# Optimization experiments

Hardware: AMD Instinct MI355X
Metric: run time of the kernel (lower is better)

## Reference

```python
import jax, jax.numpy as jnp
import numpy as np
from jax import lax

SIGMA = 3.0
AP_CUT = 15


def _gauss_kernel(sigma, truncate=4.0):
    r = int(truncate * sigma + 0.5)
    x = np.arange(-r, r + 1, dtype=np.float32)
    k = np.exp(-0.5 * (x / sigma) ** 2)
    return jnp.asarray(k / k.sum()), r

KERN, RAD = _gauss_kernel(SIGMA)


def _smooth(f):
    """Separable Gaussian smoothing; circular on y (DV), replicate on x (AP).
    f: [..., Y, X] -> same shape."""
    lead = f.shape[:-2]
    Y, X = f.shape[-2:]
    g = f.reshape((-1, 1, Y, X))
    g = jnp.pad(g, ((0, 0), (0, 0), (RAD, RAD), (0, 0)), mode='wrap')
    g = jnp.pad(g, ((0, 0), (0, 0), (0, 0), (RAD, RAD)), mode='edge')
    ky = KERN.reshape(1, 1, -1, 1)
    kx = KERN.reshape(1, 1, 1, -1)
    g = lax.conv_general_dilated(g, ky, (1, 1), 'VALID')
    g = lax.conv_general_dilated(g, kx, (1, 1), 'VALID')
    return g.reshape(lead + (Y, X))


def _gradient(f):
    """Covariant gradient: Gaussian smooth then central differences.
    Returns [..., Y, X, 2] with index 0 = d/dy (circular), 1 = d/dx (replicate)."""
    g = _smooth(f)
    dy = 0.5 * (jnp.roll(g, -1, axis=-2) - jnp.roll(g, 1, axis=-2))
    gp = jnp.pad(g, [(0, 0)] * (g.ndim - 1) + [(1, 1)], mode='edge')
    dx = 0.5 * (gp[..., 2:] - gp[..., :-2])
    return jnp.stack([dy, dx], axis=-1)


def _postprocess(f):
    f = f.at[..., :AP_CUT].set(0.0)
    f = f.at[..., -AP_CUT:].set(0.0)
    return _smooth(f)


def setup_inputs() -> dict:
    key = jax.random.key(0)
    k1, k2 = jax.random.split(key)
    Y, X = 1024, 2048
    y = 0.1 * jax.random.normal(k1, (5, Y, X), dtype=jnp.float32)
    v = 0.1 * jax.random.normal(k2, (2, Y, X), dtype=jnp.float32)
    return {"y": y, "v": v}


def reference(y, v):
    Y, X = y.shape[-2:]
    # InputProcessor.transform: split state into 2x2 tensor m and scalar s
    m = y[:4].reshape(2, 2, Y, X)
    s = y[4]

    # get_velocity: left-right symmetrization (flip DV axis, negate y-component)
    v_lr = jnp.flip(v, axis=-2)
    v_lr = v_lr.at[0].multiply(-1.0)
    v = 0.5 * (v + v_lr)

    d1_m = _gradient(m)          # [2,2,Y,X,2]
    d1_s = _gradient(s)          # [Y,X,2]
    d1_v = _gradient(v)          # [2,Y,X,2]

    sdot = -jnp.einsum('iyx,yxi->yx', v, d1_s)

    T = jnp.transpose(d1_v, (0, 3, 1, 2))       # iyxj -> ijyx
    Tt = jnp.transpose(T, (1, 0, 2, 3))
    O = -0.5 * (T - Tt)                         # vorticity
    E = 0.5 * (T + Tt)                          # strain rate

    lhs = jnp.einsum('kyx,ijyxk->ijyx', v, d1_m)
    lhs = lhs + jnp.einsum('ikyx,kjyx->ijyx', O, m)
    lhs = lhs - jnp.einsum('ikyx,kjyx->ijyx', m, O)

    # rhs_eCad reaction terms
    trm = jnp.einsum('kkyx->yx', m)
    trE = jnp.einsum('kkyx->yx', E)
    gamma_dv = jnp.array([[1.0, 0.0], [0.0, 0.0]], dtype=y.dtype)[..., None, None]
    rhs = -(0.11 - 0.099 * s) * m
    rhs = rhs + (0.767 + 0.055 * s) * m * trE
    rhs = rhs + (0.732 - 0.59 * s) * trm * m
    rhs = rhs + (0.069 - 0.048 * s) * trm * gamma_dv

    mdot = _postprocess(-lhs + rhs)
    sdot = _postprocess(sdot)

    # inverse_transform: stack back into 5-channel state derivative
    return jnp.concatenate([mdot.reshape(4, Y, X), sdot[None]], axis=0)
```

## Files before the change

### kernel.cpp

```cpp
#include <hip/hip_runtime.h>
#include <math.h>

#define Y_ 1024
#define X_ 2048
#define YX_ (Y_*X_)
#define RAD_ 12
#define NT_ 25
#define ND_ 27
#define APC_ 15
#define PAD_ 16

struct W25 { float w[NT_]; };
struct D27 { float d[ND_]; };

__global__ __launch_bounds__(256) void ksmooth_y7c(
    const float* __restrict__ yin, const float* __restrict__ vin,
    float* __restrict__ out, W25 W)
{
  const int id = blockIdx.x;
  const int w  = (id & 7) * 112 + (id >> 3);
  const int yg = w % 64, xh = (w / 64) & 1, z = w / 128;
  const int y0 = yg * 16;
  const int xo = xh * 1024 + threadIdx.x * 4;

  float4 acc[16];
#pragma unroll
  for (int j = 0; j < 16; ++j) acc[j] = make_float4(0.f, 0.f, 0.f, 0.f);

  if (z < 5) {
    const float* base = yin + z * YX_;
#pragma unroll
    for (int g = 0; g < 4; ++g) {
      float4 b[10];
#pragma unroll
      for (int i = 0; i < 10; ++i) {
        const int r = (y0 - RAD_ + 10*g + i + Y_) & (Y_ - 1);
        b[i] = *(const float4*)(base + r * X_ + xo);
      }
#pragma unroll
      for (int i = 0; i < 10; ++i) {
        const int t = 10*g + i;
#pragma unroll
        for (int j = 0; j < 16; ++j) {
          const int k = t - j;
          if (k >= 0 && k < NT_) {
            const float wk = W.w[k];
            acc[j].x += wk * b[i].x; acc[j].y += wk * b[i].y;
            acc[j].z += wk * b[i].z; acc[j].w += wk * b[i].w;
          }
        }
      }
    }
  } else {
    const int   c   = z - 5;
    const float sgn = (c == 0) ? -1.f : 1.f;
    const float* base = vin + c * YX_;
#pragma unroll
    for (int g = 0; g < 8; ++g) {
      float4 a5[5], b5[5];
#pragma unroll
      for (int i = 0; i < 5; ++i) {
        const int r = (y0 - RAD_ + 5*g + i + Y_) & (Y_ - 1);
        a5[i] = *(const float4*)(base + r * X_ + xo);
        b5[i] = *(const float4*)(base + (Y_ - 1 - r) * X_ + xo);
      }
#pragma unroll
      for (int i = 0; i < 5; ++i) {
        const int t = 5*g + i;
        float4 val;
        val.x = 0.5f * (a5[i].x + sgn * b5[i].x);
        val.y = 0.5f * (a5[i].y + sgn * b5[i].y);
        val.z = 0.5f * (a5[i].z + sgn * b5[i].z);
        val.w = 0.5f * (a5[i].w + sgn * b5[i].w);
#pragma unroll
        for (int j = 0; j < 16; ++j) {
          const int k = t - j;
          if (k >= 0 && k < NT_) {
            const float wk = W.w[k];
            acc[j].x += wk * val.x; acc[j].y += wk * val.y;
            acc[j].z += wk * val.z; acc[j].w += wk * val.w;
          }
        }
      }
    }
  }
#pragma unroll
  for (int j = 0; j < 16; ++j)
    *(float4*)(out + z * YX_ + (y0 + j) * X_ + xo) = acc[j];
}

__device__ __forceinline__ void stage_row(
    float (&slot)[4][264], const float* __restrict__ src, int tid)
{
  float4 v = *(const float4*)(src + 4 * tid);
  slot[0][tid] = v.x; slot[1][tid] = v.y; slot[2][tid] = v.z; slot[3][tid] = v.w;
  if (tid < 8) {
    float4 v2 = *(const float4*)(src + 1024 + 4 * tid);
    slot[0][256+tid] = v2.x; slot[1][256+tid] = v2.y;
    slot[2][256+tid] = v2.z; slot[3][256+tid] = v2.w;
  }
}

__device__ __forceinline__ void conv_lds(
    const float (&L)[3][4][264], int tid, const W25& W, const D27& D,
    float dX[4], float dY[4])
{
#pragma unroll
  for (int j = 0; j < 4; ++j) { dX[j] = 0.f; dY[j] = 0.f; }
#pragma unroll
  for (int i = 3; i <= 33; ++i) {
    const float v = L[1][i & 3][tid + (i >> 2)];
#pragma unroll
    for (int j = 0; j < 4; ++j) {
      const int k = i - 3 - j;
      if (k >= 0 && k < ND_) dX[j] += D.d[k] * v;
    }
  }
#pragma unroll
  for (int i = 4; i <= 31; ++i) {
    const float u = L[2][i & 3][tid + (i >> 2)];
    const float d = L[0][i & 3][tid + (i >> 2)];
    const float dv = 0.5f * (u - d);
#pragma unroll
    for (int j = 0; j < 4; ++j) {
      const int k = i - 4 - j;
      if (k >= 0 && k < NT_) dY[j] += W.w[k] * dv;
    }
  }
}

__global__ __launch_bounds__(256, 4) void kfused_lds3(
    const float* __restrict__ gY,
    const float* __restrict__ yin,
    const float* __restrict__ vin,
    float* __restrict__ B,
    W25 W, D27 D)
{
  __shared__ float lds[3][4][264];
  const int tid = threadIdx.x;
  const int id  = blockIdx.x;
  const int w   = (id & 7) * 256 + (id >> 3);
  const int yy  = w & (Y_ - 1);
  const int xh  = w >> 10;
  const int xb  = xh * 1024;
  const int x0  = xb + 4 * tid;
  const int yu  = (yy + 1) & (Y_ - 1);
  const int yd  = (yy - 1) & (Y_ - 1);

  float v0[4], v1[4];
  {
    float4 a = *(const float4*)(vin + 0 * YX_ + yy * X_ + x0);
    float4 b = *(const float4*)(vin + 0 * YX_ + (Y_ - 1 - yy) * X_ + x0);
    float4 c = *(const float4*)(vin + 1 * YX_ + yy * X_ + x0);
    float4 d = *(const float4*)(vin + 1 * YX_ + (Y_ - 1 - yy) * X_ + x0);
    v0[0] = 0.5f*(a.x-b.x); v0[1] = 0.5f*(a.y-b.y);
    v0[2] = 0.5f*(a.z-b.z); v0[3] = 0.5f*(a.w-b.w);
    v1[0] = 0.5f*(c.x+d.x); v1[1] = 0.5f*(c.y+d.y);
    v1[2] = 0.5f*(c.z+d.z); v1[3] = 0.5f*(c.w+d.w);
  }

  float dXa[4], dYa[4], w_[4], trE[4];
  float ac0[4], ac1[4], ac2[4], ac3[4], ac4[4];

  {
    const float* b5 = gY + 5 * YX_;
    stage_row(lds[0], b5 + yd * X_ + xb - 16, tid);
    stage_row(lds[1], b5 + yy * X_ + xb - 16, tid);
    stage_row(lds[2], b5 + yu * X_ + xb - 16, tid);
  }
  __syncthreads();

#pragma unroll 1
  for (int ci = 0; ci < 7; ++ci) {
    float dX[4], dY[4];
    conv_lds(lds, tid, W, D, dX, dY);
    switch (ci) {
      case 0:
#pragma unroll
        for (int j = 0; j < 4; ++j) { dXa[j] = dX[j]; dYa[j] = dY[j]; }
        break;
      case 1:
#pragma unroll
        for (int j = 0; j < 4; ++j) {
          w_[j]  = -0.5f * (dXa[j] - dY[j]);
          trE[j] = dYa[j] + dX[j];
        }
        break;
      case 2:
#pragma unroll
        for (int j = 0; j < 4; ++j) ac0[j] = v0[j]*dY[j] + v1[j]*dX[j];
        break;
      case 3:
#pragma unroll
        for (int j = 0; j < 4; ++j) ac1[j] = v0[j]*dY[j] + v1[j]*dX[j];
        break;
      case 4:
#pragma unroll
        for (int j = 0; j < 4; ++j) ac2[j] = v0[j]*dY[j] + v1[j]*dX[j];
        break;
      case 5:
#pragma unroll
        for (int j = 0; j < 4; ++j) ac3[j] = v0[j]*dY[j] + v1[j]*dX[j];
        break;
      default:
#pragma unroll
        for (int j = 0; j < 4; ++j) ac4[j] = v0[j]*dY[j] + v1[j]*dX[j];
        break;
    }
    if (ci < 6) {
      __syncthreads();
      const int nch = (ci == 0) ? 6 : ci - 1;
      const float* bn = gY + nch * YX_;
      stage_row(lds[0], bn + yd * X_ + xb - 16, tid);
      stage_row(lds[1], bn + yy * X_ + xb - 16, tid);
      stage_row(lds[2], bn + yu * X_ + xb - 16, tid);
      __syncthreads();
    }
  }

  float rm[5][4];
#pragma unroll
  for (int zc = 0; zc < 5; ++zc) {
    float4 t = *(const float4*)(yin + zc * YX_ + yy * X_ + x0);
    rm[zc][0] = t.x; rm[zc][1] = t.y; rm[zc][2] = t.z; rm[zc][3] = t.w;
  }

  float o[5][4];
#pragma unroll
  for (int j = 0; j < 4; ++j) {
    const float m00r = rm[0][j], m01r = rm[1][j], m10r = rm[2][j], m11r = rm[3][j];
    const float sr   = rm[4][j];
    const float wj   = w_[j];
    const float trm  = m00r + m11r;

    const float lhs00 = ac0[j] + wj * (m10r + m01r);
    const float lhs01 = ac1[j] + wj * (m11r - m00r);
    const float lhs10 = ac2[j] + wj * (m11r - m00r);
    const float lhs11 = ac3[j] - wj * (m01r + m10r);

    const float f  = -(0.11f - 0.099f * sr)
                   + (0.767f + 0.055f * sr) * trE[j]
                   + (0.732f - 0.59f  * sr) * trm;
    const float cd = (0.069f - 0.048f * sr) * trm;
    const float sd = -ac4[j];

    const int   xg   = x0 + j;
    const float mask = (xg < APC_ || xg >= X_ - APC_) ? 0.f : 1.f;
    o[0][j] = mask * (f * m00r + cd - lhs00);
    o[1][j] = mask * (f * m01r      - lhs01);
    o[2][j] = mask * (f * m10r      - lhs10);
    o[3][j] = mask * (f * m11r      - lhs11);
    o[4][j] = mask * sd;
  }
#pragma unroll
  for (int zc = 0; zc < 5; ++zc)
    *(float4*)(B + zc * YX_ + yy * X_ + x0) =
        make_float4(o[zc][0], o[zc][1], o[zc][2], o[zc][3]);
}

__global__ __launch_bounds__(256) void kxsmooth(
    const float* __restrict__ in, float* __restrict__ out, W25 W)
{
  const int z  = blockIdx.z;
  const int yy = blockIdx.y;
  const int x0 = (blockIdx.x * 256 + threadIdx.x) * 4;
  const float* row = in + z * YX_ + yy * X_;

  float buf[28];
  if (x0 >= RAD_ && x0 + 4 + RAD_ <= X_) {
#pragma unroll
    for (int i = 0; i < 7; ++i) {
      float4 t = *(const float4*)(row + x0 - RAD_ + 4 * i);
      buf[4*i+0] = t.x; buf[4*i+1] = t.y; buf[4*i+2] = t.z; buf[4*i+3] = t.w;
    }
  } else {
#pragma unroll
    for (int i = 0; i < 28; ++i) {
      int xx = x0 - RAD_ + i;
      xx = xx < 0 ? 0 : (xx > X_ - 1 ? X_ - 1 : xx);
      buf[i] = row[xx];
    }
  }
  float a0 = 0.f, a1 = 0.f, a2 = 0.f, a3 = 0.f;
#pragma unroll
  for (int t = 0; t < NT_; ++t) {
    const float wk = W.w[t];
    a0 += wk * buf[t + 0];
    a1 += wk * buf[t + 1];
    a2 += wk * buf[t + 2];
    a3 += wk * buf[t + 3];
  }
  *(float4*)(out + z * YX_ + yy * X_ + x0) = make_float4(a0, a1, a2, a3);
}

__global__ __launch_bounds__(256) void ksmooth_y5c(
    const float* __restrict__ in, float* __restrict__ out, W25 W)
{
  const int id = blockIdx.x;
  const int w  = (id & 7) * 80 + (id >> 3);
  const int yg = w % 64, xh = (w / 64) & 1, z = w / 128;
  const int y0 = yg * 16;
  const int xo = xh * 1024 + threadIdx.x * 4;
  const float* base = in + z * YX_;

  float4 acc[16];
#pragma unroll
  for (int j = 0; j < 16; ++j) acc[j] = make_float4(0.f, 0.f, 0.f, 0.f);

#pragma unroll
  for (int g = 0; g < 4; ++g) {
    float4 b[10];
#pragma unroll
    for (int i = 0; i < 10; ++i) {
      const int r = (y0 - RAD_ + 10*g + i + Y_) & (Y_ - 1);
      b[i] = *(const float4*)(base + r * X_ + xo);
    }
#pragma unroll
    for (int i = 0; i < 10; ++i) {
      const int t = 10*g + i;
#pragma unroll
      for (int j = 0; j < 16; ++j) {
        const int k = t - j;
        if (k >= 0 && k < NT_) {
          const float wk = W.w[k];
          acc[j].x += wk * b[i].x; acc[j].y += wk * b[i].y;
          acc[j].z += wk * b[i].z; acc[j].w += wk * b[i].w;
        }
      }
    }
  }
#pragma unroll
  for (int j = 0; j < 16; ++j)
    *(float4*)(out + z * YX_ + (y0 + j) * X_ + xo) = acc[j];
}

extern "C" void kernel_launch(void* const* d_in, const int* in_sizes, int n_in,
                              void* d_out, int out_size, void* d_ws, size_t ws_size,
                              hipStream_t stream)
{
  const float* yin = (const float*)d_in[0];
  const float* vin = (const float*)d_in[1];
  float* out = (float*)d_out;

  float* gY = (float*)d_ws + PAD_;
  float* B  = gY + 7 * (size_t)YX_;
  float* C  = gY;

  W25 W; D27 D;
  double wd[NT_], s = 0.0;
  for (int i = 0; i < NT_; ++i) {
    const double x = i - RAD_;
    wd[i] = exp(-0.5 * (x / 3.0) * (x / 3.0));
    s += wd[i];
  }
  for (int i = 0; i < NT_; ++i) W.w[i] = (float)(wd[i] / s);
  for (int t = 0; t < ND_; ++t) {
    const double a = (t - 2 >= 0 && t - 2 < NT_) ? wd[t - 2] / s : 0.0;
    const double b = (t < NT_) ? wd[t] / s : 0.0;
    D.d[t] = (float)(0.5 * (a - b));
  }

  ksmooth_y7c<<<896,  256, 0, stream>>>(yin, vin, gY, W);
  kfused_lds3<<<2048, 256, 0, stream>>>(gY, yin, vin, B, W, D);
  kxsmooth   <<<dim3(2, 1024, 5), 256, 0, stream>>>(B, C, W);
  ksmooth_y5c<<<640,  256, 0, stream>>>(C, out, W);
}
```

Measured before the change: 226.3 us.

## Fuse x-direction smoothing into gradient kernel with halo recompute and double-buffered LDS

```diff
diff --git a/kernel.cpp b/kernel.cpp
--- a/kernel.cpp
+++ b/kernel.cpp
@@ -8,7 +8,7 @@
 #define NT_ 25
 #define ND_ 27
 #define APC_ 15
-#define PAD_ 16
+#define PAD_ 32
 
 struct W25 { float w[NT_]; };
 struct D27 { float d[ND_]; };
@@ -89,27 +89,24 @@
     *(float4*)(out + z * YX_ + (y0 + j) * X_ + xo) = acc[j];
 }
 
-__device__ __forceinline__ void stage_row(
-    float (&slot)[4][264], const float* __restrict__ src, int tid)
-{
-  float4 v = *(const float4*)(src + 4 * tid);
-  slot[0][tid] = v.x; slot[1][tid] = v.y; slot[2][tid] = v.z; slot[3][tid] = v.w;
-  if (tid < 8) {
-    float4 v2 = *(const float4*)(src + 1024 + 4 * tid);
-    slot[0][256+tid] = v2.x; slot[1][256+tid] = v2.y;
-    slot[2][256+tid] = v2.z; slot[3][256+tid] = v2.w;
-  }
-}
-
-__device__ __forceinline__ void conv_lds(
-    const float (&L)[3][4][264], int tid, const W25& W, const D27& D,
+__device__ __forceinline__ void stage_row2(
+    float (&slot)[4][272], const float* __restrict__ src, int tid)
+{
+  if (tid < 270) {
+    float4 v = *(const float4*)(src + 4 * tid);
+    slot[0][tid] = v.x; slot[1][tid] = v.y; slot[2][tid] = v.z; slot[3][tid] = v.w;
+  }
+}
+
+__device__ __forceinline__ void conv_lds2(
+    const float (&L)[3][4][272], int g, const W25& W, const D27& D,
     float dX[4], float dY[4])
 {
 #pragma unroll
   for (int j = 0; j < 4; ++j) { dX[j] = 0.f; dY[j] = 0.f; }
 #pragma unroll
   for (int i = 3; i <= 33; ++i) {
-    const float v = L[1][i & 3][tid + (i >> 2)];
+    const float v = L[1][i & 3][g + (i >> 2)];
 #pragma unroll
     for (int j = 0; j < 4; ++j) {
       const int k = i - 3 - j;
@@ -118,8 +115,8 @@
   }
 #pragma unroll
   for (int i = 4; i <= 31; ++i) {
-    const float u = L[2][i & 3][tid + (i >> 2)];
-    const float d = L[0][i & 3][tid + (i >> 2)];
+    const float u = L[2][i & 3][g + (i >> 2)];
+    const float d = L[0][i & 3][g + (i >> 2)];
     const float dv = 0.5f * (u - d);
 #pragma unroll
     for (int j = 0; j < 4; ++j) {
@@ -129,30 +126,33 @@
   }
 }
 
-__global__ __launch_bounds__(256, 4) void kfused_lds3(
+__global__ __launch_bounds__(320, 3) void kfused_x(
     const float* __restrict__ gY,
     const float* __restrict__ yin,
     const float* __restrict__ vin,
-    float* __restrict__ B,
+    float* __restrict__ Bx,
     W25 W, D27 D)
 {
-  __shared__ float lds[3][4][264];
+  __shared__ float lds[2][3][4][272];
+  __shared__ float ox[5][4][264];
   const int tid = threadIdx.x;
   const int id  = blockIdx.x;
   const int w   = (id & 7) * 256 + (id >> 3);
   const int yy  = w & (Y_ - 1);
   const int xh  = w >> 10;
   const int xb  = xh * 1024;
-  const int x0  = xb + 4 * tid;
+  const int x0  = xb - 12 + 4 * tid;
   const int yu  = (yy + 1) & (Y_ - 1);
   const int yd  = (yy - 1) & (Y_ - 1);
+  const bool act = (tid < 262);
+  const int xr  = x0 < 0 ? 0 : (x0 > X_ - 4 ? X_ - 4 : x0);
 
   float v0[4], v1[4];
   {
-    float4 a = *(const float4*)(vin + 0 * YX_ + yy * X_ + x0);
-    float4 b = *(const float4*)(vin + 0 * YX_ + (Y_ - 1 - yy) * X_ + x0);
-    float4 c = *(const float4*)(vin + 1 * YX_ + yy * X_ + x0);
-    float4 d = *(const float4*)(vin + 1 * YX_ + (Y_ - 1 - yy) * X_ + x0);
+    float4 a = *(const float4*)(vin + 0 * YX_ + yy * X_ + xr);
+    float4 b = *(const float4*)(vin + 0 * YX_ + (Y_ - 1 - yy) * X_ + xr);
+    float4 c = *(const float4*)(vin + 1 * YX_ + yy * X_ + xr);
+    float4 d = *(const float4*)(vin + 1 * YX_ + (Y_ - 1 - yy) * X_ + xr);
     v0[0] = 0.5f*(a.x-b.x); v0[1] = 0.5f*(a.y-b.y);
     v0[2] = 0.5f*(a.z-b.z); v0[3] = 0.5f*(a.w-b.w);
     v1[0] = 0.5f*(c.x+d.x); v1[1] = 0.5f*(c.y+d.y);
@@ -164,16 +164,24 @@
 
   {
     const float* b5 = gY + 5 * YX_;
-    stage_row(lds[0], b5 + yd * X_ + xb - 16, tid);
-    stage_row(lds[1], b5 + yy * X_ + xb - 16, tid);
-    stage_row(lds[2], b5 + yu * X_ + xb - 16, tid);
+    stage_row2(lds[0][0], b5 + yd * X_ + xb - 28, tid);
+    stage_row2(lds[0][1], b5 + yy * X_ + xb - 28, tid);
+    stage_row2(lds[0][2], b5 + yu * X_ + xb - 28, tid);
   }
   __syncthreads();
 
 #pragma unroll 1
   for (int ci = 0; ci < 7; ++ci) {
+    if (ci < 6) {
+      const int nch = (ci == 0) ? 6 : ci - 1;
+      const float* bn = gY + nch * YX_;
+      float (&nb)[3][4][272] = lds[(ci + 1) & 1];
+      stage_row2(nb[0], bn + yd * X_ + xb - 28, tid);
+      stage_row2(nb[1], bn + yy * X_ + xb - 28, tid);
+      stage_row2(nb[2], bn + yu * X_ + xb - 28, tid);
+    }
     float dX[4], dY[4];
-    conv_lds(lds, tid, W, D, dX, dY);
+    conv_lds2(lds[ci & 1], act ? tid : 0, W, D, dX, dY);
     switch (ci) {
       case 0:
 #pragma unroll
@@ -207,90 +215,67 @@
         for (int j = 0; j < 4; ++j) ac4[j] = v0[j]*dY[j] + v1[j]*dX[j];
         break;
     }
-    if (ci < 6) {
-      __syncthreads();
-      const int nch = (ci == 0) ? 6 : ci - 1;
-      const float* bn = gY + nch * YX_;
-      stage_row(lds[0], bn + yd * X_ + xb - 16, tid);
-      stage_row(lds[1], bn + yy * X_ + xb - 16, tid);
-      stage_row(lds[2], bn + yu * X_ + xb - 16, tid);
-      __syncthreads();
-    }
-  }
-
-  float rm[5][4];
-#pragma unroll
-  for (int zc = 0; zc < 5; ++zc) {
-    float4 t = *(const float4*)(yin + zc * YX_ + yy * X_ + x0);
-    rm[zc][0] = t.x; rm[zc][1] = t.y; rm[zc][2] = t.z; rm[zc][3] = t.w;
-  }
-
-  float o[5][4];
-#pragma unroll
-  for (int j = 0; j < 4; ++j) {
-    const float m00r = rm[0][j], m01r = rm[1][j], m10r = rm[2][j], m11r = rm[3][j];
-    const float sr   = rm[4][j];
-    const float wj   = w_[j];
-    const float trm  = m00r + m11r;
-
-    const float lhs00 = ac0[j] + wj * (m10r + m01r);
-    const float lhs01 = ac1[j] + wj * (m11r - m00r);
-    const float lhs10 = ac2[j] + wj * (m11r - m00r);
-    const float lhs11 = ac3[j] - wj * (m01r + m10r);
-
-    const float f  = -(0.11f - 0.099f * sr)
-                   + (0.767f + 0.055f * sr) * trE[j]
-                   + (0.732f - 0.59f  * sr) * trm;
-    const float cd = (0.069f - 0.048f * sr) * trm;
-    const float sd = -ac4[j];
-
-    const int   xg   = x0 + j;
-    const float mask = (xg < APC_ || xg >= X_ - APC_) ? 0.f : 1.f;
-    o[0][j] = mask * (f * m00r + cd - lhs00);
-    o[1][j] = mask * (f * m01r      - lhs01);
-    o[2][j] = mask * (f * m10r      - lhs10);
-    o[3][j] = mask * (f * m11r      - lhs11);
-    o[4][j] = mask * sd;
-  }
-#pragma unroll
-  for (int zc = 0; zc < 5; ++zc)
-    *(float4*)(B + zc * YX_ + yy * X_ + x0) =
-        make_float4(o[zc][0], o[zc][1], o[zc][2], o[zc][3]);
-}
-
-__global__ __launch_bounds__(256) void kxsmooth(
-    const float* __restrict__ in, float* __restrict__ out, W25 W)
-{
-  const int z  = blockIdx.z;
-  const int yy = blockIdx.y;
-  const int x0 = (blockIdx.x * 256 + threadIdx.x) * 4;
-  const float* row = in + z * YX_ + yy * X_;
-
-  float buf[28];
-  if (x0 >= RAD_ && x0 + 4 + RAD_ <= X_) {
-#pragma unroll
-    for (int i = 0; i < 7; ++i) {
-      float4 t = *(const float4*)(row + x0 - RAD_ + 4 * i);
-      buf[4*i+0] = t.x; buf[4*i+1] = t.y; buf[4*i+2] = t.z; buf[4*i+3] = t.w;
-    }
-  } else {
-#pragma unroll
-    for (int i = 0; i < 28; ++i) {
-      int xx = x0 - RAD_ + i;
-      xx = xx < 0 ? 0 : (xx > X_ - 1 ? X_ - 1 : xx);
-      buf[i] = row[xx];
-    }
-  }
-  float a0 = 0.f, a1 = 0.f, a2 = 0.f, a3 = 0.f;
-#pragma unroll
-  for (int t = 0; t < NT_; ++t) {
-    const float wk = W.w[t];
-    a0 += wk * buf[t + 0];
-    a1 += wk * buf[t + 1];
-    a2 += wk * buf[t + 2];
-    a3 += wk * buf[t + 3];
-  }
-  *(float4*)(out + z * YX_ + yy * X_ + x0) = make_float4(a0, a1, a2, a3);
+    __syncthreads();
+  }
+
+  if (act) {
+    float rm[5][4];
+#pragma unroll
+    for (int zc = 0; zc < 5; ++zc) {
+      float4 t = *(const float4*)(yin + zc * YX_ + yy * X_ + xr);
+      rm[zc][0] = t.x; rm[zc][1] = t.y; rm[zc][2] = t.z; rm[zc][3] = t.w;
+    }
+#pragma unroll
+    for (int j = 0; j < 4; ++j) {
+      const float m00r = rm[0][j], m01r = rm[1][j], m10r = rm[2][j], m11r = rm[3][j];
+      const float sr   = rm[4][j];
+      const float wj   = w_[j];
+      const float trm  = m00r + m11r;
+
+      const float lhs00 = ac0[j] + wj * (m10r + m01r);
+      const float lhs01 = ac1[j] + wj * (m11r - m00r);
+      const float lhs10 = ac2[j] + wj * (m11r - m00r);
+      const float lhs11 = ac3[j] - wj * (m01r + m10r);
+
+      const float f  = -(0.11f - 0.099f * sr)
+                     + (0.767f + 0.055f * sr) * trE[j]
+                     + (0.732f - 0.59f  * sr) * trm;
+      const float cd = (0.069f - 0.048f * sr) * trm;
+      const float sd = -ac4[j];
+
+      const int   xg   = x0 + j;
+      const float mask = (xg < APC_ || xg >= X_ - APC_) ? 0.f : 1.f;
+      ox[0][j][tid] = mask * (f * m00r + cd - lhs00);
+      ox[1][j][tid] = mask * (f * m01r      - lhs01);
+      ox[2][j][tid] = mask * (f * m10r      - lhs10);
+      ox[3][j][tid] = mask * (f * m11r      - lhs11);
+      ox[4][j][tid] = mask * sd;
+    }
+  }
+  __syncthreads();
+
+  if (tid < 256) {
+#pragma unroll
+    for (int zc = 0; zc < 5; ++zc) {
+      float a0 = 0.f, a1 = 0.f, a2 = 0.f, a3 = 0.f;
+#pragma unroll
+      for (int i = 0; i < 28; ++i) {
+        const float v = ox[zc][i & 3][tid + (i >> 2)];
+#pragma unroll
+        for (int j = 0; j < 4; ++j) {
+          const int k = i - j;
+          if (k >= 0 && k < NT_) {
+            if (j == 0) a0 += W.w[k] * v;
+            if (j == 1) a1 += W.w[k] * v;
+            if (j == 2) a2 += W.w[k] * v;
+            if (j == 3) a3 += W.w[k] * v;
+          }
+        }
+      }
+      *(float4*)(Bx + zc * YX_ + yy * X_ + xb + 4 * tid) =
+          make_float4(a0, a1, a2, a3);
+    }
+  }
 }
 
 __global__ __launch_bounds__(256) void ksmooth_y5c(
@@ -343,8 +328,7 @@
   float* out = (float*)d_out;
 
   float* gY = (float*)d_ws + PAD_;
-  float* B  = gY + 7 * (size_t)YX_;
-  float* C  = gY;
+  float* Bx = gY + 7 * (size_t)YX_;
 
   W25 W; D27 D;
   double wd[NT_], s = 0.0;
@@ -361,7 +345,6 @@
   }
 
   ksmooth_y7c<<<896,  256, 0, stream>>>(yin, vin, gY, W);
-  kfused_lds3<<<2048, 256, 0, stream>>>(gY, yin, vin, B, W, D);
-  kxsmooth   <<<dim3(2, 1024, 5), 256, 0, stream>>>(B, C, W);
-  ksmooth_y5c<<<640,  256, 0, stream>>>(C, out, W);
-}
+  kfused_x   <<<2048, 320, 0, stream>>>(gY, yin, vin, Bx, W, D);
+  ksmooth_y5c<<<640,  256, 0, stream>>>(Bx, out, W);
+}
```

New measurement: 241.5 us. 6.7% more time.
